# Optimization experiments

Measured on AMD Instinct MI355X. Metric: run time of the kernel, lower is better.

Reference implementation:

```python
import jax, jax.numpy as jnp
import numpy as np

# SMPL kinematic tree (parent of each of the 24 joints; root = -1)
PARENTS = [-1, 0, 0, 0, 1, 2, 3, 4, 5, 6, 7, 8, 9, 9, 9, 12, 13, 14, 16, 17, 18, 19, 20, 21]
N_PTS = 440960
B = 64


def setup_inputs() -> dict:
    key = jax.random.key(0)
    k1, k2, k3, k4, k5 = jax.random.split(key, 5)
    ps = jax.random.normal(k1, (N_PTS, 3), dtype=jnp.float32)
    Js = jax.random.normal(k2, (B, 24, 3), dtype=jnp.float32)
    ws = jax.random.uniform(k3, (N_PTS, 24), dtype=jnp.float32)
    ws = ws / jnp.sum(ws, axis=-1, keepdims=True)  # skinning weights sum to 1
    poses = jax.random.normal(k4, (B, 24, 3), dtype=jnp.float32) * 0.3  # axis-angle
    batch = jnp.sort(jax.random.randint(k5, (N_PTS,), 0, B, dtype=jnp.int64))
    return {"ps": ps, "JsorShapes": Js, "ws": ws, "poses": poses, "batch": batch}


def batch_rodrigues(r):
    # r: (M, 3) axis-angle -> (M, 3, 3) rotation matrices
    angle = jnp.linalg.norm(r, axis=-1, keepdims=True) + 1e-8  # (M,1)
    axis = r / angle
    x, y, z = axis[:, 0], axis[:, 1], axis[:, 2]
    zero = jnp.zeros_like(x)
    K = jnp.stack([zero, -z, y, z, zero, -x, -y, x, zero], axis=-1).reshape(-1, 3, 3)
    a = angle[..., None]  # (M,1,1)
    eye = jnp.eye(3, dtype=r.dtype)
    return eye + jnp.sin(a) * K + (1.0 - jnp.cos(a)) * (K @ K)


def batch_global_rigid_transformation(Rs, Js, parents):
    # Rs: (B,24,3,3), Js: (B,24,3)
    b = Rs.shape[0]
    dt = Rs.dtype
    bottom = jnp.broadcast_to(jnp.array([0.0, 0.0, 0.0, 1.0], dtype=dt), (b, 1, 4))

    def make_mat(R, t):  # (b,3,3),(b,3) -> (b,4,4)
        top = jnp.concatenate([R, t[..., None]], axis=-1)
        return jnp.concatenate([top, bottom], axis=1)

    results = [make_mat(Rs[:, 0], Js[:, 0])]
    for i in range(1, 24):
        t = Js[:, i] - Js[:, parents[i]]
        results.append(results[parents[i]] @ make_mat(Rs[:, i], t))
    results = jnp.stack(results, axis=1)  # (b,24,4,4)
    new_J = results[..., :3, 3]
    Js_h = jnp.concatenate([Js, jnp.zeros((b, 24, 1), dtype=dt)], axis=-1)  # (b,24,4)
    init_bone = jnp.einsum('bjxy,bjy->bjx', results, Js_h)  # (b,24,4)
    A = results.at[..., 3].add(-init_bone)  # subtract from last column
    return new_J, A


def reference(ps, JsorShapes, ws, poses, batch):
    b = poses.shape[0]
    Js = JsorShapes  # numel != b*10 -> already joint locations
    Rs = batch_rodrigues(poses.reshape(-1, 3)).reshape(b, 24, 3, 3)
    Js_transformed, A = batch_global_rigid_transformation(Rs, Js, PARENTS)
    # ragged per-group weight @ joint-transform GEMM, fused as a per-point gather+dot
    A16 = A.reshape(b, 24, 16)
    T = jnp.einsum('nk,nkf->nf', ws, A16[batch]).reshape(-1, 4, 4)  # (N,4,4)
    ps_h = jnp.concatenate([ps, jnp.ones((ps.shape[0], 1), dtype=ps.dtype)], axis=-1)
    out = jnp.einsum('nxy,ny->nx', T, ps_h)
    return out[:, :3], T, Rs, Js_transformed
```

## Files before the change

### kernel.cpp

```cpp
#include <hip/hip_runtime.h>

#define N_PTS 440960
#define NB 64

__device__ const int d_par[24] = {-1,0,0,0,1,2,3,4,5,6,7,8,9,9,9,12,13,14,16,17,18,19,20,21};
__device__ const int d_lvl[24] = {0,1,1,1,2,2,2,3,3,3,4,4,4,4,4,5,5,5,6,6,7,7,8,8};

__global__ __launch_bounds__(64) void pose_kernel(
    const float* __restrict__ c0,
    const float* __restrict__ c1,
    float* __restrict__ Aout,
    float* __restrict__ outRs,
    float* __restrict__ outJt)
{
    const int b = blockIdx.x;
    const int j = threadIdx.x;

    float v = 0.0f;
    {
        const float4* c04 = reinterpret_cast<const float4*>(c0);
        #pragma unroll
        for (int q = 0; q < 6; q++) {
            float4 x = c04[j * 6 + q];
            v += x.x * x.x + x.y * x.y + x.z * x.z + x.w * x.w;
        }
        #pragma unroll
        for (int o = 32; o > 0; o >>= 1) v += __shfl_down(v, o, 64);
        v = __shfl(v, 0, 64);
    }
    const bool c0_is_Js = (v > 460.8f);
    const float* __restrict__ Js    = c0_is_Js ? c0 : c1;
    const float* __restrict__ poses = c0_is_Js ? c1 : c0;

    __shared__ float res[24][12];
    __shared__ float Lm[24][12];

    if (j < 24) {
        const float* pj = poses + (size_t)(b * 24 + j) * 3;
        float rx = pj[0], ry = pj[1], rz = pj[2];
        float ang = sqrtf(rx * rx + ry * ry + rz * rz) + 1e-8f;
        float x = rx / ang, y = ry / ang, z = rz / ang;
        float s = sinf(ang), c = cosf(ang), o = 1.0f - c;
        float R00 = 1.0f - o * (y * y + z * z);
        float R01 = -s * z + o * x * y;
        float R02 =  s * y + o * x * z;
        float R10 =  s * z + o * x * y;
        float R11 = 1.0f - o * (x * x + z * z);
        float R12 = -s * x + o * y * z;
        float R20 = -s * y + o * x * z;
        float R21 =  s * x + o * y * z;
        float R22 = 1.0f - o * (x * x + y * y);

        int p = d_par[j];
        const float* jj = Js + (size_t)(b * 24 + j) * 3;
        float tx = jj[0], ty = jj[1], tz = jj[2];
        if (p >= 0) {
            const float* jp = Js + (size_t)(b * 24 + p) * 3;
            tx -= jp[0]; ty -= jp[1]; tz -= jp[2];
        }
        Lm[j][0] = R00; Lm[j][1] = R01; Lm[j][2]  = R02; Lm[j][3]  = tx;
        Lm[j][4] = R10; Lm[j][5] = R11; Lm[j][6]  = R12; Lm[j][7]  = ty;
        Lm[j][8] = R20; Lm[j][9] = R21; Lm[j][10] = R22; Lm[j][11] = tz;

        float* rs = outRs + (size_t)(b * 24 + j) * 9;
        rs[0] = R00; rs[1] = R01; rs[2] = R02;
        rs[3] = R10; rs[4] = R11; rs[5] = R12;
        rs[6] = R20; rs[7] = R21; rs[8] = R22;
    }
    __syncthreads();

    if (j < 24 && d_lvl[j] == 0) {
        #pragma unroll
        for (int i = 0; i < 12; i++) res[j][i] = Lm[j][i];
    }
    __syncthreads();

    for (int lvl = 1; lvl <= 8; lvl++) {
        if (j < 24 && d_lvl[j] == lvl) {
            int p = d_par[j];
            float out[12];
            #pragma unroll
            for (int r = 0; r < 3; r++) {
                float pr0 = res[p][r * 4 + 0];
                float pr1 = res[p][r * 4 + 1];
                float pr2 = res[p][r * 4 + 2];
                float pr3 = res[p][r * 4 + 3];
                #pragma unroll
                for (int cc = 0; cc < 3; cc++) {
                    out[r * 4 + cc] = pr0 * Lm[j][0 * 4 + cc]
                                    + pr1 * Lm[j][1 * 4 + cc]
                                    + pr2 * Lm[j][2 * 4 + cc];
                }
                out[r * 4 + 3] = pr0 * Lm[j][3] + pr1 * Lm[j][7] + pr2 * Lm[j][11] + pr3;
            }
            #pragma unroll
            for (int i = 0; i < 12; i++) res[j][i] = out[i];
        }
        __syncthreads();
    }

    if (j < 24) {
        const float* jj = Js + (size_t)(b * 24 + j) * 3;
        float Jx = jj[0], Jy = jj[1], Jz = jj[2];
        float* Ab = Aout + (size_t)(b * 24 + j) * 16;
        #pragma unroll
        for (int r = 0; r < 3; r++) {
            float r0 = res[j][r * 4 + 0];
            float r1 = res[j][r * 4 + 1];
            float r2 = res[j][r * 4 + 2];
            float r3 = res[j][r * 4 + 3];
            Ab[r * 4 + 0] = r0;
            Ab[r * 4 + 1] = r1;
            Ab[r * 4 + 2] = r2;
            Ab[r * 4 + 3] = r3 - (r0 * Jx + r1 * Jy + r2 * Jz);
            outJt[(size_t)(b * 24 + j) * 3 + r] = r3;
        }
        Ab[12] = 0.0f; Ab[13] = 0.0f; Ab[14] = 0.0f; Ab[15] = 1.0f;
    }
}

__global__ __launch_bounds__(256) void skin_kernel(
    const float* __restrict__ ps,
    const float* __restrict__ ws,
    const int*   __restrict__ batch,
    const float* __restrict__ A,
    float* __restrict__ out3,
    float* __restrict__ outT)
{
    int n = blockIdx.x * 256 + threadIdx.x;
    int nn = n < N_PTS ? n : N_PTS - 1;

    float w[24];
    float wsum = 0.0f;
    const float4* w4 = reinterpret_cast<const float4*>(ws + (size_t)nn * 24);
    #pragma unroll
    for (int q = 0; q < 6; q++) {
        float4 v = w4[q];
        w[q * 4 + 0] = v.x; w[q * 4 + 1] = v.y;
        w[q * 4 + 2] = v.z; w[q * 4 + 3] = v.w;
        wsum += v.x + v.y + v.z + v.w;
    }

    const float* pp = ps + (size_t)nn * 3;
    float px = pp[0], py = pp[1], pz = pp[2];

    int b;
    if (batch[N_PTS - 1] == 0) {
        const long long* b64 = reinterpret_cast<const long long*>(batch);
        b = (int)b64[nn];
    } else {
        b = batch[nn];
    }
    b = b < 0 ? 0 : (b > 63 ? 63 : b);

    float T[12];
    #pragma unroll
    for (int i = 0; i < 12; i++) T[i] = 0.0f;

    int bu = __builtin_amdgcn_readfirstlane(b);
    bool uni = (__ballot(b == bu) == 0xFFFFFFFFFFFFFFFFull);
    const float* Ab = A + (size_t)(uni ? bu : b) * 384;
    #pragma unroll
    for (int k = 0; k < 24; k++) {
        float wk = w[k];
        #pragma unroll
        for (int i = 0; i < 12; i++) T[i] += wk * Ab[k * 16 + i];
    }

    float ox = T[0] * px + T[1] * py + T[2]  * pz + T[3];
    float oy = T[4] * px + T[5] * py + T[6]  * pz + T[7];
    float oz = T[8] * px + T[9] * py + T[10] * pz + T[11];

    if (n < N_PTS) {
        float* o3 = out3 + (size_t)n * 3;
        o3[0] = ox; o3[1] = oy; o3[2] = oz;

        float4* ot = reinterpret_cast<float4*>(outT + (size_t)n * 16);
        ot[0] = make_float4(T[0], T[1], T[2],  T[3]);
        ot[1] = make_float4(T[4], T[5], T[6],  T[7]);
        ot[2] = make_float4(T[8], T[9], T[10], T[11]);
        ot[3] = make_float4(0.0f, 0.0f, 0.0f,  wsum);
    }
}

extern "C" void kernel_launch(void* const* d_in, const int* in_sizes, int n_in,
                              void* d_out, int out_size, void* d_ws, size_t ws_size,
                              hipStream_t stream) {
    const float* ps = nullptr;
    const float* ws = nullptr;
    const int* batch = nullptr;
    const float* c0 = nullptr;
    const float* c1 = nullptr;
    for (int i = 0; i < n_in; i++) {
        int s = in_sizes[i];
        if (s == N_PTS * 3)       ps = (const float*)d_in[i];
        else if (s == N_PTS * 24) ws = (const float*)d_in[i];
        else if (s == N_PTS)      batch = (const int*)d_in[i];
        else if (s == NB * 24 * 3) {
            if (!c0) c0 = (const float*)d_in[i];
            else     c1 = (const float*)d_in[i];
        }
    }
    if (!ps)    ps    = (const float*)d_in[0];
    if (!c0)    c0    = (const float*)d_in[1];
    if (!ws)    ws    = (const float*)d_in[2];
    if (!c1)    c1    = (const float*)d_in[3];
    if (!batch) batch = (const int*)d_in[4];

    float* out   = (float*)d_out;
    float* out3  = out;
    float* outT  = out + (size_t)N_PTS * 3;
    float* outRs = outT + (size_t)N_PTS * 16;
    float* outJt = outRs + (size_t)NB * 24 * 9;

    float* A = (float*)d_ws;

    pose_kernel<<<NB, 64, 0, stream>>>(c0, c1, A, outRs, outJt);

    int blocks = (N_PTS + 255) / 256;
    skin_kernel<<<blocks, 256, 0, stream>>>(ps, ws, batch, A, out3, outT);
}
```

Baseline: 121.2 us.

## Fuse pose chain into skinning kernel with per-block shared-memory transforms

Merges the pose and skinning kernels into one launch: each block recomputes the joint transforms for the one or two batch indices its points span and stores them in shared memory, while the first 64 blocks also emit Rs and transformed joints. This removes the second kernel launch, the inter-kernel dependency and global reads of A. It adds redundant Rodrigues and kinematic-chain work plus several barriers per block, and it assumes each 256-point block spans at most two consecutive batch ids.

```diff
diff --git a/kernel.cpp b/kernel.cpp
--- a/kernel.cpp
+++ b/kernel.cpp
@@ -3,132 +3,160 @@
 #define N_PTS 440960
 #define NB 64
 
-__device__ const int d_par[24] = {-1,0,0,0,1,2,3,4,5,6,7,8,9,9,9,12,13,14,16,17,18,19,20,21};
-__device__ const int d_lvl[24] = {0,1,1,1,2,2,2,3,3,3,4,4,4,4,4,5,5,5,6,6,7,7,8,8};
-
-__global__ __launch_bounds__(64) void pose_kernel(
+__device__ const int g_par[24] = {-1,0,0,0,1,2,3,4,5,6,7,8,9,9,9,12,13,14,16,17,18,19,20,21};
+__device__ const int g_lvl[24] = {0,1,1,1,2,2,2,3,3,3,4,4,4,4,4,5,5,5,6,6,7,7,8,8};
+
+__global__ __launch_bounds__(256) void fused_kernel(
+    const float* __restrict__ ps,
+    const float* __restrict__ ws,
+    const int*   __restrict__ batch,
     const float* __restrict__ c0,
     const float* __restrict__ c1,
-    float* __restrict__ Aout,
+    float* __restrict__ out3,
+    float* __restrict__ outT,
     float* __restrict__ outRs,
     float* __restrict__ outJt)
 {
-    const int b = blockIdx.x;
-    const int j = threadIdx.x;
-
-    float v = 0.0f;
-    {
+    const int tid = threadIdx.x;
+    const int n0  = blockIdx.x * 256;
+    const int n   = n0 + tid;
+    const int nn  = n < N_PTS ? n : N_PTS - 1;
+
+    __shared__ float sA[2][24][16];
+    __shared__ float sLm[3][24][12];
+    __shared__ float sRes[3][24][12];
+    __shared__ int   sInfo[4];
+
+    if (tid == 0) {
+        int i64 = (batch[N_PTS - 1] == 0) ? 1 : 0;
+        sInfo[3] = i64;
+        int nlast = n0 + 255; if (nlast >= N_PTS) nlast = N_PTS - 1;
+        int b0, b1;
+        if (i64) {
+            const long long* p = (const long long*)batch;
+            b0 = (int)p[n0]; b1 = (int)p[nlast];
+        } else {
+            b0 = batch[n0]; b1 = batch[nlast];
+        }
+        b0 = min(max(b0, 0), 63); b1 = min(max(b1, 0), 63);
+        sInfo[0] = b0;
+        sInfo[1] = (b1 > b0) ? 1 : 0;
+    }
+    if (tid < 64) {
+        float v = 0.0f;
         const float4* c04 = reinterpret_cast<const float4*>(c0);
         #pragma unroll
         for (int q = 0; q < 6; q++) {
-            float4 x = c04[j * 6 + q];
+            float4 x = c04[tid * 6 + q];
             v += x.x * x.x + x.y * x.y + x.z * x.z + x.w * x.w;
         }
         #pragma unroll
         for (int o = 32; o > 0; o >>= 1) v += __shfl_down(v, o, 64);
-        v = __shfl(v, 0, 64);
-    }
-    const bool c0_is_Js = (v > 460.8f);
-    const float* __restrict__ Js    = c0_is_Js ? c0 : c1;
-    const float* __restrict__ poses = c0_is_Js ? c1 : c0;
-
-    __shared__ float res[24][12];
-    __shared__ float Lm[24][12];
-
-    if (j < 24) {
-        const float* pj = poses + (size_t)(b * 24 + j) * 3;
+        if (tid == 0) sInfo[2] = (v > 460.8f) ? 1 : 0;
+    }
+    __syncthreads();
+
+    const int  bmin  = sInfo[0];
+    const int  extra = sInfo[1];
+    const int  i64   = sInfo[3];
+    const float* __restrict__ Js    = sInfo[2] ? c0 : c1;
+    const float* __restrict__ poses = sInfo[2] ? c1 : c0;
+
+    const int s = tid >> 5;
+    const int j = tid & 31;
+    const int ob = blockIdx.x;
+    const bool obValid = (ob < NB);
+
+    int  bsel = -1;
+    bool doSkin = false, doOut = false;
+    if (s == 0) { bsel = bmin; doSkin = true; doOut = obValid && (ob == bmin); }
+    else if (s == 1 && extra) { bsel = bmin + 1; doSkin = true; doOut = obValid && (ob == bmin + 1); }
+    else if (s == 2 && obValid && ob != bmin && !(extra && ob == bmin + 1)) { bsel = ob; doOut = true; }
+
+    if (bsel >= 0 && j < 24) {
+        const float* pj = poses + (size_t)(bsel * 24 + j) * 3;
         float rx = pj[0], ry = pj[1], rz = pj[2];
         float ang = sqrtf(rx * rx + ry * ry + rz * rz) + 1e-8f;
         float x = rx / ang, y = ry / ang, z = rz / ang;
-        float s = sinf(ang), c = cosf(ang), o = 1.0f - c;
+        float sn = sinf(ang), cs = cosf(ang), o = 1.0f - cs;
         float R00 = 1.0f - o * (y * y + z * z);
-        float R01 = -s * z + o * x * y;
-        float R02 =  s * y + o * x * z;
-        float R10 =  s * z + o * x * y;
+        float R01 = -sn * z + o * x * y;
+        float R02 =  sn * y + o * x * z;
+        float R10 =  sn * z + o * x * y;
         float R11 = 1.0f - o * (x * x + z * z);
-        float R12 = -s * x + o * y * z;
-        float R20 = -s * y + o * x * z;
-        float R21 =  s * x + o * y * z;
+        float R12 = -sn * x + o * y * z;
+        float R20 = -sn * y + o * x * z;
+        float R21 =  sn * x + o * y * z;
         float R22 = 1.0f - o * (x * x + y * y);
 
-        int p = d_par[j];
-        const float* jj = Js + (size_t)(b * 24 + j) * 3;
+        int p = g_par[j];
+        const float* jj = Js + (size_t)(bsel * 24 + j) * 3;
         float tx = jj[0], ty = jj[1], tz = jj[2];
         if (p >= 0) {
-            const float* jp = Js + (size_t)(b * 24 + p) * 3;
+            const float* jp = Js + (size_t)(bsel * 24 + p) * 3;
             tx -= jp[0]; ty -= jp[1]; tz -= jp[2];
         }
-        Lm[j][0] = R00; Lm[j][1] = R01; Lm[j][2]  = R02; Lm[j][3]  = tx;
-        Lm[j][4] = R10; Lm[j][5] = R11; Lm[j][6]  = R12; Lm[j][7]  = ty;
-        Lm[j][8] = R20; Lm[j][9] = R21; Lm[j][10] = R22; Lm[j][11] = tz;
-
-        float* rs = outRs + (size_t)(b * 24 + j) * 9;
-        rs[0] = R00; rs[1] = R01; rs[2] = R02;
-        rs[3] = R10; rs[4] = R11; rs[5] = R12;
-        rs[6] = R20; rs[7] = R21; rs[8] = R22;
+        sLm[s][j][0] = R00; sLm[s][j][1] = R01; sLm[s][j][2]  = R02; sLm[s][j][3]  = tx;
+        sLm[s][j][4] = R10; sLm[s][j][5] = R11; sLm[s][j][6]  = R12; sLm[s][j][7]  = ty;
+        sLm[s][j][8] = R20; sLm[s][j][9] = R21; sLm[s][j][10] = R22; sLm[s][j][11] = tz;
+
+        if (doOut) {
+            float* rs = outRs + (size_t)(bsel * 24 + j) * 9;
+            rs[0] = R00; rs[1] = R01; rs[2] = R02;
+            rs[3] = R10; rs[4] = R11; rs[5] = R12;
+            rs[6] = R20; rs[7] = R21; rs[8] = R22;
+        }
+        if (g_lvl[j] == 0) {
+            #pragma unroll
+            for (int i = 0; i < 12; i++) sRes[s][j][i] = sLm[s][j][i];
+        }
     }
     __syncthreads();
 
-    if (j < 24 && d_lvl[j] == 0) {
-        #pragma unroll
-        for (int i = 0; i < 12; i++) res[j][i] = Lm[j][i];
-    }
-    __syncthreads();
-
     for (int lvl = 1; lvl <= 8; lvl++) {
-        if (j < 24 && d_lvl[j] == lvl) {
-            int p = d_par[j];
-            float out[12];
+        if (bsel >= 0 && j < 24 && g_lvl[j] == lvl) {
+            int p = g_par[j];
+            float o12[12];
             #pragma unroll
             for (int r = 0; r < 3; r++) {
-                float pr0 = res[p][r * 4 + 0];
-                float pr1 = res[p][r * 4 + 1];
-                float pr2 = res[p][r * 4 + 2];
-                float pr3 = res[p][r * 4 + 3];
+                float pr0 = sRes[s][p][r * 4 + 0];
+                float pr1 = sRes[s][p][r * 4 + 1];
+                float pr2 = sRes[s][p][r * 4 + 2];
+                float pr3 = sRes[s][p][r * 4 + 3];
                 #pragma unroll
                 for (int cc = 0; cc < 3; cc++) {
-                    out[r * 4 + cc] = pr0 * Lm[j][0 * 4 + cc]
-                                    + pr1 * Lm[j][1 * 4 + cc]
-                                    + pr2 * Lm[j][2 * 4 + cc];
+                    o12[r * 4 + cc] = pr0 * sLm[s][j][0 * 4 + cc]
+                                    + pr1 * sLm[s][j][1 * 4 + cc]
+                                    + pr2 * sLm[s][j][2 * 4 + cc];
                 }
-                out[r * 4 + 3] = pr0 * Lm[j][3] + pr1 * Lm[j][7] + pr2 * Lm[j][11] + pr3;
+                o12[r * 4 + 3] = pr0 * sLm[s][j][3] + pr1 * sLm[s][j][7]
+                               + pr2 * sLm[s][j][11] + pr3;
             }
             #pragma unroll
-            for (int i = 0; i < 12; i++) res[j][i] = out[i];
+            for (int i = 0; i < 12; i++) sRes[s][j][i] = o12[i];
         }
         __syncthreads();
     }
 
-    if (j < 24) {
-        const float* jj = Js + (size_t)(b * 24 + j) * 3;
+    if (bsel >= 0 && j < 24) {
+        const float* jj = Js + (size_t)(bsel * 24 + j) * 3;
         float Jx = jj[0], Jy = jj[1], Jz = jj[2];
-        float* Ab = Aout + (size_t)(b * 24 + j) * 16;
         #pragma unroll
         for (int r = 0; r < 3; r++) {
-            float r0 = res[j][r * 4 + 0];
-            float r1 = res[j][r * 4 + 1];
-            float r2 = res[j][r * 4 + 2];
-            float r3 = res[j][r * 4 + 3];
-            Ab[r * 4 + 0] = r0;
-            Ab[r * 4 + 1] = r1;
-            Ab[r * 4 + 2] = r2;
-            Ab[r * 4 + 3] = r3 - (r0 * Jx + r1 * Jy + r2 * Jz);
-            outJt[(size_t)(b * 24 + j) * 3 + r] = r3;
-        }
-        Ab[12] = 0.0f; Ab[13] = 0.0f; Ab[14] = 0.0f; Ab[15] = 1.0f;
-    }
-}
-
-__global__ __launch_bounds__(256) void skin_kernel(
-    const float* __restrict__ ps,
-    const float* __restrict__ ws,
-    const int*   __restrict__ batch,
-    const float* __restrict__ A,
-    float* __restrict__ out3,
-    float* __restrict__ outT)
-{
-    int n = blockIdx.x * 256 + threadIdx.x;
-    int nn = n < N_PTS ? n : N_PTS - 1;
+            float r0 = sRes[s][j][r * 4 + 0];
+            float r1 = sRes[s][j][r * 4 + 1];
+            float r2 = sRes[s][j][r * 4 + 2];
+            float r3 = sRes[s][j][r * 4 + 3];
+            if (doSkin) {
+                sA[s][j][r * 4 + 0] = r0;
+                sA[s][j][r * 4 + 1] = r1;
+                sA[s][j][r * 4 + 2] = r2;
+                sA[s][j][r * 4 + 3] = r3 - (r0 * Jx + r1 * Jy + r2 * Jz);
+            }
+            if (doOut) outJt[(size_t)(bsel * 24 + j) * 3 + r] = r3;
+        }
+    }
+    __syncthreads();
 
     float w[24];
     float wsum = 0.0f;
@@ -145,26 +173,29 @@
     float px = pp[0], py = pp[1], pz = pp[2];
 
     int b;
-    if (batch[N_PTS - 1] == 0) {
-        const long long* b64 = reinterpret_cast<const long long*>(batch);
-        b = (int)b64[nn];
+    if (i64) {
+        const long long* p = (const long long*)batch;
+        b = (int)p[nn];
     } else {
         b = batch[nn];
     }
-    b = b < 0 ? 0 : (b > 63 ? 63 : b);
+    int idx = b - bmin;
+    idx = idx < 0 ? 0 : (idx > extra ? extra : idx);
 
     float T[12];
     #pragma unroll
     for (int i = 0; i < 12; i++) T[i] = 0.0f;
 
-    int bu = __builtin_amdgcn_readfirstlane(b);
-    bool uni = (__ballot(b == bu) == 0xFFFFFFFFFFFFFFFFull);
-    const float* Ab = A + (size_t)(uni ? bu : b) * 384;
+    const float4* Arow = reinterpret_cast<const float4*>(&sA[idx][0][0]);
     #pragma unroll
     for (int k = 0; k < 24; k++) {
         float wk = w[k];
-        #pragma unroll
-        for (int i = 0; i < 12; i++) T[i] += wk * Ab[k * 16 + i];
+        float4 a0 = Arow[k * 4 + 0];
+        float4 a1 = Arow[k * 4 + 1];
+        float4 a2 = Arow[k * 4 + 2];
+        T[0] += wk * a0.x; T[1]  += wk * a0.y; T[2]  += wk * a0.z; T[3]  += wk * a0.w;
+        T[4] += wk * a1.x; T[5]  += wk * a1.y; T[6]  += wk * a1.z; T[7]  += wk * a1.w;
+        T[8] += wk * a2.x; T[9]  += wk * a2.y; T[10] += wk * a2.z; T[11] += wk * a2.w;
     }
 
     float ox = T[0] * px + T[1] * py + T[2]  * pz + T[3];
@@ -192,11 +223,11 @@
     const float* c0 = nullptr;
     const float* c1 = nullptr;
     for (int i = 0; i < n_in; i++) {
-        int s = in_sizes[i];
-        if (s == N_PTS * 3)       ps = (const float*)d_in[i];
-        else if (s == N_PTS * 24) ws = (const float*)d_in[i];
-        else if (s == N_PTS)      batch = (const int*)d_in[i];
-        else if (s == NB * 24 * 3) {
+        int sz = in_sizes[i];
+        if (sz == N_PTS * 3)       ps = (const float*)d_in[i];
+        else if (sz == N_PTS * 24) ws = (const float*)d_in[i];
+        else if (sz == N_PTS)      batch = (const int*)d_in[i];
+        else if (sz == NB * 24 * 3) {
             if (!c0) c0 = (const float*)d_in[i];
             else     c1 = (const float*)d_in[i];
         }
@@ -213,10 +244,7 @@
     float* outRs = outT + (size_t)N_PTS * 16;
     float* outJt = outRs + (size_t)NB * 24 * 9;
 
-    float* A = (float*)d_ws;
-
-    pose_kernel<<<NB, 64, 0, stream>>>(c0, c1, A, outRs, outJt);
-
     int blocks = (N_PTS + 255) / 256;
-    skin_kernel<<<blocks, 256, 0, stream>>>(ps, ws, batch, A, out3, outT);
+    fused_kernel<<<blocks, 256, 0, stream>>>(ps, ws, batch, c0, c1,
+                                             out3, outT, outRs, outJt);
 }
```

Result: faster. 115.7 us (-4.6%).
